# Kernel optimization log

Measured on AMD Instinct MI355X. Metric: run time of the kernel, lower is better.

## Reference

```python
import jax, jax.numpy as jnp
import numpy as np

N_NODES = 50000
N_EDGES = 600000
IN_DIM = 128
OUT_DIM = 1024


def setup_inputs() -> dict:
    key = jax.random.key(0)
    k1, k2, k3 = jax.random.split(key, 3)
    x = jax.random.normal(k1, (N_NODES, IN_DIM), dtype=jnp.float32)
    edge_index = jax.random.randint(k2, (2, N_EDGES), 0, N_NODES, dtype=jnp.int64)
    # Linear(3*in_dim, out_dim): weight stored as [3*in_dim, out_dim] for x @ W
    W = jax.random.normal(k3, (3 * IN_DIM, OUT_DIM), dtype=jnp.float32) * (1.0 / np.sqrt(3 * IN_DIM))
    b = jnp.zeros((OUT_DIM,), dtype=jnp.float32)
    return {"x": x, "edge_index": edge_index, "W": W, "b": b}


def _mean_aggregate(feats, seg_ids, n):
    # segment-mean: sum gathered features per segment, divide by count (>=1)
    s = jax.ops.segment_sum(feats, seg_ids, num_segments=n)          # [N, d]
    cnt = jax.ops.segment_sum(jnp.ones((feats.shape[0],), feats.dtype), seg_ids, num_segments=n)
    return s / jnp.maximum(cnt, 1.0)[:, None]


def reference(x, edge_index, W, b):
    n = x.shape[0]
    src = edge_index[0]
    dst = edge_index[1]
    # mean over in-neighbors (messages flow src -> dst)
    mean_in = _mean_aggregate(x[src], dst, n)
    # mean over out-neighbors (messages flow dst -> src)
    mean_out = _mean_aggregate(x[dst], src, n)
    h = jnp.concatenate([x, mean_in, mean_out], axis=-1)             # [N, 3*in_dim]
    return jax.nn.relu(h @ W + b)                                    # [N, out_dim]
```

## Files before the change

### kernel.cpp

```cpp
#include <hip/hip_runtime.h>
#include <hip/hip_bf16.h>


typedef __attribute__((ext_vector_type(8))) short bf16x8;
typedef __attribute__((ext_vector_type(4))) short bf16x4;
typedef __attribute__((ext_vector_type(4))) float f32x4;

#define IN_DIM 128
#define AGG 256
#define K3 384
#define ODIM 1024

static __device__ inline short bfs(float f) {
    union { __hip_bfloat16 b; short s; } u;
    u.b = __float2bfloat16(f);
    return u.s;
}

__global__ __launch_bounds__(256) void sage_prep(
    const float* __restrict__ x, const int* __restrict__ src,
    const int* __restrict__ dst, const float* __restrict__ W,
    __hip_bfloat16* __restrict__ xb, __hip_bfloat16* __restrict__ Wt,
    int* __restrict__ deg, int n_nodes, int n_edges, int wtB, int convB)
{
    int b = blockIdx.x;
    int t = threadIdx.x;
    if (b < wtB) {
        __shared__ __hip_bfloat16 lds[32][36];
        int tk = b / 32, tn = b % 32;
        int k0 = tk * 32, n0 = tn * 32;
        int r = t >> 3, c = (t & 7) * 4;
        f32x4 w = *(const f32x4*)(W + (size_t)(k0 + r) * ODIM + n0 + c);
#pragma unroll
        for (int i = 0; i < 4; ++i) lds[c + i][r] = __float2bfloat16(w[i]);
        __syncthreads();
        *(bf16x4*)&Wt[(size_t)(n0 + r) * K3 + k0 + c] = *(bf16x4*)&lds[r][c];
        return;
    }
    b -= wtB;
    if (b < convB) {
        int tid = b * 256 + t;
        if (tid >= n_nodes * 16) return;
        int i = tid >> 4, d8 = (tid & 15) << 3;
        const float* xp = x + (size_t)i * IN_DIM + d8;
        f32x4 a = *(const f32x4*)xp;
        f32x4 c4 = *(const f32x4*)(xp + 4);
        bf16x8 v;
        v[0] = bfs(a.x); v[1] = bfs(a.y); v[2] = bfs(a.z); v[3] = bfs(a.w);
        v[4] = bfs(c4.x); v[5] = bfs(c4.y); v[6] = bfs(c4.z); v[7] = bfs(c4.w);
        *(bf16x8*)(xb + (size_t)i * IN_DIM + d8) = v;
        return;
    }
    b -= convB;
    int e = b * 256 + t;
    if (e >= 2 * n_edges) return;
    int idx = (e < n_edges) ? dst[e] : n_nodes + src[e - n_edges];
    atomicAdd(deg + idx, 1);
}

__global__ __launch_bounds__(256) void scan_partial(
    const int* __restrict__ deg, int* __restrict__ off, int* __restrict__ bsum, int n)
{
    __shared__ int s[256];
    int t = threadIdx.x;
    int base = blockIdx.x * 1024 + t * 4;
    int4 v = {0, 0, 0, 0};
    if (base + 3 < n) v = *(const int4*)(deg + base);
    else {
        if (base     < n) v.x = deg[base];
        if (base + 1 < n) v.y = deg[base + 1];
        if (base + 2 < n) v.z = deg[base + 2];
        if (base + 3 < n) v.w = deg[base + 3];
    }
    int tsum = v.x + v.y + v.z + v.w;
    s[t] = tsum;
    __syncthreads();
#pragma unroll
    for (int d = 1; d < 256; d <<= 1) {
        int add = (t >= d) ? s[t - d] : 0;
        __syncthreads();
        s[t] += add;
        __syncthreads();
    }
    int excl = s[t] - tsum;
    if (t == 255) bsum[blockIdx.x] = s[255];
    int e0 = excl, e1 = e0 + v.x, e2 = e1 + v.y, e3 = e2 + v.z;
    if (base     < n) off[base]     = e0;
    if (base + 1 < n) off[base + 1] = e1;
    if (base + 2 < n) off[base + 2] = e2;
    if (base + 3 < n) off[base + 3] = e3;
}

__global__ __launch_bounds__(256) void scan_bsum(int* __restrict__ bsum, int nblk)
{
    __shared__ int s[256];
    int t = threadIdx.x;
    int v = (t < nblk) ? bsum[t] : 0;
    s[t] = v;
    __syncthreads();
#pragma unroll
    for (int d = 1; d < 256; d <<= 1) {
        int add = (t >= d) ? s[t - d] : 0;
        __syncthreads();
        s[t] += add;
        __syncthreads();
    }
    if (t < nblk) bsum[t] = s[t] - v;
}

__global__ __launch_bounds__(256) void scan_add(
    int* __restrict__ off, int* __restrict__ cursor,
    const int* __restrict__ bsum, int n)
{
    int base = blockIdx.x * 1024 + threadIdx.x * 4;
    int b = bsum[blockIdx.x];
#pragma unroll
    for (int j = 0; j < 4; ++j)
        if (base + j < n) {
            int v = off[base + j] + b;
            off[base + j]    = v;
            cursor[base + j] = v;
        }
}

__global__ __launch_bounds__(256) void sage_fill(
    const int* __restrict__ src, const int* __restrict__ dst,
    int* __restrict__ cursor, int* __restrict__ csr, int n_nodes, int n_edges)
{
    int t = blockIdx.x * 256 + threadIdx.x;
    if (t >= 2 * n_edges) return;
    int node, val;
    if (t < n_edges) { node = dst[t]; val = src[t]; }
    else { int e = t - n_edges; node = n_nodes + src[e]; val = dst[e]; }
    int p = atomicAdd(cursor + node, 1);
    csr[p] = val;
}

__global__ __launch_bounds__(256) void sage_aggregate(
    const __hip_bfloat16* __restrict__ xb, const int* __restrict__ csr,
    const int* __restrict__ off, const int* __restrict__ deg,
    __hip_bfloat16* __restrict__ hagg, int n_nodes)
{
    int wid  = (int)((blockIdx.x * 256 + threadIdx.x) >> 6);
    int lane = threadIdx.x & 63;
    if (wid >= 2 * n_nodes) return;
    int i = wid >> 1;
    int d = wid & 1;
    int idx = i + d * n_nodes;

    float2 a = {0.f, 0.f};
    int b0 = off[idx], dg = deg[idx];
    const int* cp = csr + b0;

#define GATHER(nb) { \
    __hip_bfloat162 v = ((const __hip_bfloat162*)(xb + (size_t)(nb) * IN_DIM))[lane]; \
    a.x += __low2float(v); a.y += __high2float(v); }

    int e = 0;
    for (; e + 7 < dg; e += 8) {
        int a0 = cp[e],     a1 = cp[e + 1], a2 = cp[e + 2], a3 = cp[e + 3];
        int a4 = cp[e + 4], a5 = cp[e + 5], a6 = cp[e + 6], a7 = cp[e + 7];
        GATHER(a0) GATHER(a1) GATHER(a2) GATHER(a3)
        GATHER(a4) GATHER(a5) GATHER(a6) GATHER(a7)
    }
    for (; e + 3 < dg; e += 4) {
        int a0 = cp[e], a1 = cp[e + 1], a2 = cp[e + 2], a3 = cp[e + 3];
        GATHER(a0) GATHER(a1) GATHER(a2) GATHER(a3)
    }
    for (; e < dg; ++e) { int a0 = cp[e]; GATHER(a0) }
#undef GATHER

    float inv = 1.0f / (float)max(dg, 1);
    __hip_bfloat162 p;
    p.x = __float2bfloat16(a.x * inv);
    p.y = __float2bfloat16(a.y * inv);
    ((__hip_bfloat162*)(hagg + (size_t)i * AGG))[(d << 6) + lane] = p;
}

__global__ __launch_bounds__(256, 4) void sage_gemm(
    const __hip_bfloat16* __restrict__ xb, const __hip_bfloat16* __restrict__ hagg,
    const __hip_bfloat16* __restrict__ Wt, const float* __restrict__ bias,
    float* __restrict__ out, int n_nodes)
{
    __shared__ __hip_bfloat16 Asm[2][128 * 32];
    __shared__ __hip_bfloat16 Bsm[2][128 * 32];

    int t    = threadIdx.x;
    int wave = t >> 6;
    int lane = t & 63;

    int bid = blockIdx.x;
    int sid = bid;
    if ((gridDim.x & 7) == 0) {
        int cpx = gridDim.x >> 3;
        sid = (bid & 7) * cpx + (bid >> 3);
    }
    int tn   = sid & 7;
    int tm   = sid >> 3;
    int m0   = tm * 128;
    int n0   = tn * 128;
    int wm   = wave >> 1;
    int wn   = wave & 1;
    int m    = lane & 15;
    int quad = lane >> 4;

    int srow = t >> 2;
    int seg  = t & 3;
    int g    = seg ^ (srow & 3);
    int ga0  = m0 + srow;       if (ga0 >= n_nodes) ga0 = n_nodes - 1;
    int ga1  = m0 + srow + 64;  if (ga1 >= n_nodes) ga1 = n_nodes - 1;
    const __hip_bfloat16* xA0 = xb   + (size_t)ga0 * IN_DIM + g * 8;
    const __hip_bfloat16* xA1 = xb   + (size_t)ga1 * IN_DIM + g * 8;
    const __hip_bfloat16* hA0 = hagg + (size_t)ga0 * AGG    + g * 8;
    const __hip_bfloat16* hA1 = hagg + (size_t)ga1 * AGG    + g * 8;
    const __hip_bfloat16* gB0 = Wt + (size_t)(n0 + srow) * K3 + g * 8;
    const __hip_bfloat16* gB1 = Wt + (size_t)(n0 + srow + 64) * K3 + g * 8;
    int l0 = (0 * 256 + wave * 64) * 8;
    int l1 = (1 * 256 + wave * 64) * 8;

    f32x4 acc[4][4];
#pragma unroll
    for (int s = 0; s < 4; ++s)
#pragma unroll
        for (int u = 0; u < 4; ++u) acc[s][u] = (f32x4){0.f, 0.f, 0.f, 0.f};

    __builtin_amdgcn_global_load_lds(xA0, &Asm[0][l0], 16, 0, 0);
    __builtin_amdgcn_global_load_lds(xA1, &Asm[0][l1], 16, 0, 0);
    __builtin_amdgcn_global_load_lds(gB0, &Bsm[0][l0], 16, 0, 0);
    __builtin_amdgcn_global_load_lds(gB1, &Bsm[0][l1], 16, 0, 0);

    int slot = quad ^ (m & 3);
#pragma unroll
    for (int kt = 0; kt < 12; ++kt) {
        int p = kt & 1;
        __syncthreads();
        if (kt < 11) {
            int kn = kt + 1;
            const __hip_bfloat16* pA0 = (kn < 4) ? xA0 + kn * 32 : hA0 + (kn - 4) * 32;
            const __hip_bfloat16* pA1 = (kn < 4) ? xA1 + kn * 32 : hA1 + (kn - 4) * 32;
            __builtin_amdgcn_global_load_lds(pA0, &Asm[p ^ 1][l0], 16, 0, 0);
            __builtin_amdgcn_global_load_lds(pA1, &Asm[p ^ 1][l1], 16, 0, 0);
            __builtin_amdgcn_global_load_lds(gB0 + kn * 32, &Bsm[p ^ 1][l0], 16, 0, 0);
            __builtin_amdgcn_global_load_lds(gB1 + kn * 32, &Bsm[p ^ 1][l1], 16, 0, 0);
        }
        bf16x8 a[4], b[4];
#pragma unroll
        for (int s = 0; s < 4; ++s) {
            int row = wm * 64 + s * 16 + m;
            a[s] = *(const bf16x8*)&Asm[p][row * 32 + slot * 8];
        }
#pragma unroll
        for (int u = 0; u < 4; ++u) {
            int row = wn * 64 + u * 16 + m;
            b[u] = *(const bf16x8*)&Bsm[p][row * 32 + slot * 8];
        }
#pragma unroll
        for (int s = 0; s < 4; ++s)
#pragma unroll
            for (int u = 0; u < 4; ++u)
                acc[s][u] = __builtin_amdgcn_mfma_f32_16x16x32_bf16(a[s], b[u], acc[s][u], 0, 0, 0);
    }

    float bv[4];
#pragma unroll
    for (int u = 0; u < 4; ++u) bv[u] = bias[n0 + wn * 64 + u * 16 + m];

    bool full = (m0 + 128 <= n_nodes);
    if (full) {
#pragma unroll
        for (int s = 0; s < 4; ++s) {
            int r0 = m0 + wm * 64 + s * 16 + quad * 4;
#pragma unroll
            for (int r = 0; r < 4; ++r) {
                float* orow = out + (size_t)(r0 + r) * ODIM + n0 + wn * 64 + m;
#pragma unroll
                for (int u = 0; u < 4; ++u)
                    __builtin_nontemporal_store(fmaxf(acc[s][u][r] + bv[u], 0.f), orow + u * 16);
            }
        }
    } else {
#pragma unroll
        for (int s = 0; s < 4; ++s) {
            int r0 = m0 + wm * 64 + s * 16 + quad * 4;
#pragma unroll
            for (int r = 0; r < 4; ++r) {
                if (r0 + r >= n_nodes) continue;
                float* orow = out + (size_t)(r0 + r) * ODIM + n0 + wn * 64 + m;
#pragma unroll
                for (int u = 0; u < 4; ++u)
                    __builtin_nontemporal_store(fmaxf(acc[s][u][r] + bv[u], 0.f), orow + u * 16);
            }
        }
    }
}

extern "C" void kernel_launch(void* const* d_in, const int* in_sizes, int n_in,
                              void* d_out, int out_size, void* d_ws, size_t ws_size,
                              hipStream_t stream)
{
    const float* x    = (const float*)d_in[0];
    const int*   ei   = (const int*)d_in[1];
    const float* W    = (const float*)d_in[2];
    const float* bias = (const float*)d_in[3];

    int n_nodes = in_sizes[0] / IN_DIM;
    int n_edges = in_sizes[1] / 2;
    const int* src = ei;
    const int* dst = ei + n_edges;
    int n2 = 2 * n_nodes;

    char* ws = (char*)d_ws;
    int* deg    = (int*)ws;
    int* cursor = deg + n2;
    int* off    = cursor + n2;
    int* bsum   = off + n2;
    int* csr    = bsum + 256;
    __hip_bfloat16* hagg = (__hip_bfloat16*)(csr + 2 * n_edges);
    __hip_bfloat16* Wt   = hagg + (size_t)n_nodes * AGG;
    __hip_bfloat16* xb   = Wt + (size_t)K3 * ODIM;

    hipMemsetAsync(deg, 0, (size_t)n2 * sizeof(int), stream);

    int wtB   = (K3 / 32) * (ODIM / 32);
    int convB = (n_nodes * 16 + 255) / 256;
    int degB  = (2 * n_edges + 255) / 256;
    sage_prep<<<wtB + convB + degB, 256, 0, stream>>>(
        x, src, dst, W, xb, Wt, deg, n_nodes, n_edges, wtB, convB);

    int nblk = (n2 + 1023) / 1024;
    scan_partial<<<nblk, 256, 0, stream>>>(deg, off, bsum, n2);
    scan_bsum<<<1, 256, 0, stream>>>(bsum, nblk);
    scan_add<<<nblk, 256, 0, stream>>>(off, cursor, bsum, n2);

    sage_fill<<<degB, 256, 0, stream>>>(src, dst, cursor, csr, n_nodes, n_edges);

    sage_aggregate<<<(n2 + 3) / 4, 256, 0, stream>>>(xb, csr, off, deg, hagg, n_nodes);

    int tiles_m = (n_nodes + 127) / 128;
    int blocks  = tiles_m * (ODIM / 128);
    sage_gemm<<<blocks, 256, 0, stream>>>(xb, hagg, Wt, bias, (float*)d_out, n_nodes);
}
```

Before: 465.1 us.

## Record atomic slot positions, merge scan kernels, vectorize neighbor gather

The degree-counting pass now stores each edge's atomic return value, so the fill kernel can write CSR entries at off+pos without a second round of atomics and without a cursor array. The block-sum scan is folded into the add kernel: every block redundantly rescans the block sums, which removes one launch. The aggregation kernel now reads 16-byte bf16x8 vectors, with four 16-lane groups each handling a different neighbor, and combines the groups through cross-lane shuffles. This cuts the number of memory instructions per neighbor, at the cost of an extra pos array write and read and a masked tail loop.

```diff
diff --git a/kernel.cpp b/kernel.cpp
--- a/kernel.cpp
+++ b/kernel.cpp
@@ -17,11 +17,18 @@
     return u.s;
 }
 
+static __device__ inline float bf2f(short s) {
+    union { unsigned u; float f; } c;
+    c.u = ((unsigned)(unsigned short)s) << 16;
+    return c.f;
+}
+
 __global__ __launch_bounds__(256) void sage_prep(
     const float* __restrict__ x, const int* __restrict__ src,
     const int* __restrict__ dst, const float* __restrict__ W,
     __hip_bfloat16* __restrict__ xb, __hip_bfloat16* __restrict__ Wt,
-    int* __restrict__ deg, int n_nodes, int n_edges, int wtB, int convB)
+    int* __restrict__ deg, int* __restrict__ pos,
+    int n_nodes, int n_edges, int wtB, int convB)
 {
     int b = blockIdx.x;
     int t = threadIdx.x;
@@ -55,7 +62,7 @@
     int e = b * 256 + t;
     if (e >= 2 * n_edges) return;
     int idx = (e < n_edges) ? dst[e] : n_nodes + src[e - n_edges];
-    atomicAdd(deg + idx, 1);
+    pos[e] = atomicAdd(deg + idx, 1);
 }
 
 __global__ __launch_bounds__(256) void scan_partial(
@@ -91,7 +98,8 @@
     if (base + 3 < n) off[base + 3] = e3;
 }
 
-__global__ __launch_bounds__(256) void scan_bsum(int* __restrict__ bsum, int nblk)
+__global__ __launch_bounds__(256) void scan_add(
+    int* __restrict__ off, const int* __restrict__ bsum, int n, int nblk)
 {
     __shared__ int s[256];
     int t = threadIdx.x;
@@ -105,35 +113,24 @@
         s[t] += add;
         __syncthreads();
     }
-    if (t < nblk) bsum[t] = s[t] - v;
-}
-
-__global__ __launch_bounds__(256) void scan_add(
-    int* __restrict__ off, int* __restrict__ cursor,
-    const int* __restrict__ bsum, int n)
-{
-    int base = blockIdx.x * 1024 + threadIdx.x * 4;
-    int b = bsum[blockIdx.x];
+    int b = s[blockIdx.x] - ((blockIdx.x < nblk) ? bsum[blockIdx.x] : 0);
+    int base = blockIdx.x * 1024 + t * 4;
 #pragma unroll
     for (int j = 0; j < 4; ++j)
-        if (base + j < n) {
-            int v = off[base + j] + b;
-            off[base + j]    = v;
-            cursor[base + j] = v;
-        }
+        if (base + j < n) off[base + j] += b;
 }
 
 __global__ __launch_bounds__(256) void sage_fill(
     const int* __restrict__ src, const int* __restrict__ dst,
-    int* __restrict__ cursor, int* __restrict__ csr, int n_nodes, int n_edges)
+    const int* __restrict__ off, const int* __restrict__ pos,
+    int* __restrict__ csr, int n_nodes, int n_edges)
 {
     int t = blockIdx.x * 256 + threadIdx.x;
     if (t >= 2 * n_edges) return;
     int node, val;
     if (t < n_edges) { node = dst[t]; val = src[t]; }
     else { int e = t - n_edges; node = n_nodes + src[e]; val = dst[e]; }
-    int p = atomicAdd(cursor + node, 1);
-    csr[p] = val;
+    csr[off[node] + pos[t]] = val;
 }
 
 __global__ __launch_bounds__(256) void sage_aggregate(
@@ -148,33 +145,46 @@
     int d = wid & 1;
     int idx = i + d * n_nodes;
 
-    float2 a = {0.f, 0.f};
     int b0 = off[idx], dg = deg[idx];
     const int* cp = csr + b0;
-
-#define GATHER(nb) { \
-    __hip_bfloat162 v = ((const __hip_bfloat162*)(xb + (size_t)(nb) * IN_DIM))[lane]; \
-    a.x += __low2float(v); a.y += __high2float(v); }
+    int q = lane >> 4, sub = lane & 15;
+
+    float acc[8];
+#pragma unroll
+    for (int j = 0; j < 8; ++j) acc[j] = 0.f;
+
+#define ACC8(v) { _Pragma("unroll") \
+    for (int j = 0; j < 8; ++j) acc[j] += bf2f((v)[j]); }
 
     int e = 0;
     for (; e + 7 < dg; e += 8) {
-        int a0 = cp[e],     a1 = cp[e + 1], a2 = cp[e + 2], a3 = cp[e + 3];
-        int a4 = cp[e + 4], a5 = cp[e + 5], a6 = cp[e + 6], a7 = cp[e + 7];
-        GATHER(a0) GATHER(a1) GATHER(a2) GATHER(a3)
-        GATHER(a4) GATHER(a5) GATHER(a6) GATHER(a7)
-    }
-    for (; e + 3 < dg; e += 4) {
-        int a0 = cp[e], a1 = cp[e + 1], a2 = cp[e + 2], a3 = cp[e + 3];
-        GATHER(a0) GATHER(a1) GATHER(a2) GATHER(a3)
-    }
-    for (; e < dg; ++e) { int a0 = cp[e]; GATHER(a0) }
-#undef GATHER
+        int r0 = cp[e + q];
+        int r1 = cp[e + 4 + q];
+        bf16x8 v0 = *(const bf16x8*)(xb + (size_t)r0 * IN_DIM + sub * 8);
+        bf16x8 v1 = *(const bf16x8*)(xb + (size_t)r1 * IN_DIM + sub * 8);
+        ACC8(v0) ACC8(v1)
+    }
+    for (; e < dg; e += 4) {
+        int eq = e + q;
+        int rq = cp[min(eq, dg - 1)];
+        bf16x8 v = *(const bf16x8*)(xb + (size_t)rq * IN_DIM + sub * 8);
+        if (eq < dg) ACC8(v)
+    }
+#undef ACC8
+
+#pragma unroll
+    for (int j = 0; j < 8; ++j) {
+        acc[j] += __shfl_xor(acc[j], 16);
+        acc[j] += __shfl_xor(acc[j], 32);
+    }
 
     float inv = 1.0f / (float)max(dg, 1);
-    __hip_bfloat162 p;
-    p.x = __float2bfloat16(a.x * inv);
-    p.y = __float2bfloat16(a.y * inv);
-    ((__hip_bfloat162*)(hagg + (size_t)i * AGG))[(d << 6) + lane] = p;
+    if (q == 0) {
+        bf16x8 o;
+#pragma unroll
+        for (int j = 0; j < 8; ++j) o[j] = bfs(acc[j] * inv);
+        *(bf16x8*)(hagg + (size_t)i * AGG + d * IN_DIM + sub * 8) = o;
+    }
 }
 
 __global__ __launch_bounds__(256, 4) void sage_gemm(
@@ -310,11 +320,11 @@
     int n2 = 2 * n_nodes;
 
     char* ws = (char*)d_ws;
-    int* deg    = (int*)ws;
-    int* cursor = deg + n2;
-    int* off    = cursor + n2;
-    int* bsum   = off + n2;
-    int* csr    = bsum + 256;
+    int* deg  = (int*)ws;
+    int* off  = deg + n2;
+    int* bsum = off + n2;
+    int* pos  = bsum + 256;
+    int* csr  = pos + 2 * n_edges;
     __hip_bfloat16* hagg = (__hip_bfloat16*)(csr + 2 * n_edges);
     __hip_bfloat16* Wt   = hagg + (size_t)n_nodes * AGG;
     __hip_bfloat16* xb   = Wt + (size_t)K3 * ODIM;
@@ -325,14 +335,13 @@
     int convB = (n_nodes * 16 + 255) / 256;
     int degB  = (2 * n_edges + 255) / 256;
     sage_prep<<<wtB + convB + degB, 256, 0, stream>>>(
-        x, src, dst, W, xb, Wt, deg, n_nodes, n_edges, wtB, convB);
+        x, src, dst, W, xb, Wt, deg, pos, n_nodes, n_edges, wtB, convB);
 
     int nblk = (n2 + 1023) / 1024;
     scan_partial<<<nblk, 256, 0, stream>>>(deg, off, bsum, n2);
-    scan_bsum<<<1, 256, 0, stream>>>(bsum, nblk);
-    scan_add<<<nblk, 256, 0, stream>>>(off, cursor, bsum, n2);
-
-    sage_fill<<<degB, 256, 0, stream>>>(src, dst, cursor, csr, n_nodes, n_edges);
+    scan_add<<<nblk, 256, 0, stream>>>(off, bsum, n2, nblk);
+
+    sage_fill<<<degB, 256, 0, stream>>>(src, dst, off, pos, csr, n_nodes, n_edges);
 
     sage_aggregate<<<(n2 + 3) / 4, 256, 0, stream>>>(xb, csr, off, deg, hagg, n_nodes);
 
```

Result: faster. 397.7 us (-14.5%).
